# Performance work log

Hardware: AMD Instinct MI355X
Metric: run time of the kernel (lower is better)

## Reference

```python
import jax, jax.numpy as jnp
import numpy as np

N_NODES = 50000
D_IN = 128
D_OUT = 128
E_POS = 500000
E_NEG = 100000
BN_EPS = 1e-5


def setup_inputs() -> dict:
    key = jax.random.key(0)
    k = jax.random.split(key, 4)
    x = jax.random.normal(k[0], (N_NODES, D_IN), dtype=jnp.float32)
    pos_edge_index = jax.random.randint(k[1], (2, E_POS), 0, N_NODES, dtype=jnp.int64)
    neg_edge_index = jax.random.randint(k[2], (2, E_NEG), 0, N_NODES, dtype=jnp.int64)
    W = jax.random.normal(k[3], (D_IN, D_OUT), dtype=jnp.float32) * 0.05
    b = jnp.zeros((D_OUT,), dtype=jnp.float32)
    gamma = jnp.ones((D_OUT,), dtype=jnp.float32)
    beta = jnp.zeros((D_OUT,), dtype=jnp.float32)
    return {"x": x, "pos_edge_index": pos_edge_index, "neg_edge_index": neg_edge_index,
            "W": W, "b": b, "gamma": gamma, "beta": beta}


def reference(x, pos_edge_index, neg_edge_index, W, b, gamma, beta):
    N = x.shape[0]
    # edge weights: 1 for pos edges, 0 for neg edges (as in the torch module)
    ei = jnp.concatenate([pos_edge_index, neg_edge_index], axis=1)
    w = jnp.concatenate([jnp.ones((pos_edge_index.shape[1],), x.dtype),
                         jnp.zeros((neg_edge_index.shape[1],), x.dtype)])
    # GCNConv gcn_norm: add self-loops with weight 1.0
    loop = jnp.arange(N)
    row = jnp.concatenate([ei[0], loop])
    col = jnp.concatenate([ei[1], loop])
    w = jnp.concatenate([w, jnp.ones((N,), x.dtype)])
    # symmetric degree normalization over target (col)
    deg = jax.ops.segment_sum(w, col, num_segments=N)
    dis = jnp.where(deg > 0, jax.lax.rsqrt(jnp.maximum(deg, 1e-12)), 0.0)
    norm = dis[row] * w * dis[col]  # [E_total]
    # linear transform first, then scatter-add aggregation at col
    h = x @ W  # [N, D_OUT]
    out = jax.ops.segment_sum(norm[:, None] * h[row], col, num_segments=N) + b
    # BatchNorm1d (training mode, biased batch var) + ReLU
    mean = out.mean(axis=0)
    var = out.var(axis=0)
    xhat = (out - mean) * jax.lax.rsqrt(var + BN_EPS)
    return jax.nn.relu(gamma * xhat + beta)
```

## Files before the change

kernel.cpp:

```cpp
#include <hip/hip_runtime.h>

#define D 128
#define BN_EPS 1e-5f
#define K_ELL 40
#define NB_AGG 1024

__device__ __forceinline__ unsigned bf16rne(float f) {
    unsigned u = __float_as_uint(f);
    return (u + 0x7fffu + ((u >> 16) & 1u)) >> 16;
}
__device__ __forceinline__ float bflo(unsigned p) { return __uint_as_float(p << 16); }
__device__ __forceinline__ float bfhi(unsigned p) { return __uint_as_float(p & 0xffff0000u); }

__global__ void count_fill(const int* __restrict__ prow, const int* __restrict__ pcol,
                           int* __restrict__ deg, int* __restrict__ ell,
                           int2* __restrict__ ovf, int* __restrict__ ovf_cnt, int E) {
    int e = blockIdx.x * blockDim.x + threadIdx.x;
    if (e < E) {
        int c = pcol[e];
        int r = prow[e];
        int p = atomicAdd(&deg[c], 1);
        if (p < K_ELL) {
            ell[c * K_ELL + p] = r;
        } else {
            int q = atomicAdd(ovf_cnt, 1);
            ovf[q] = make_int2(c, r);
        }
    }
}

__global__ __launch_bounds__(256) void gemm_xw(const float* __restrict__ x,
                                               const float* __restrict__ W,
                                               const int* __restrict__ deg,
                                               float* __restrict__ dis,
                                               unsigned* __restrict__ hb, int n) {
    __shared__ float xs[32][68];
    __shared__ float ws[32][128];
    int tid = threadIdx.x;
    int tx = tid & 31;
    int ty = tid >> 5;
    int row0 = blockIdx.x * 64;

    if (tid < 64) {
        int gr = row0 + tid;
        if (gr < n) dis[gr] = rsqrtf((float)deg[gr] + 1.0f);
    }

    float acc[8][4] = {};
    for (int k0 = 0; k0 < 128; k0 += 32) {
        #pragma unroll
        for (int i = 0; i < 2; i++) {
            int li = tid + i * 256;
            int r = li >> 3;
            int kq = li & 7;
            int grow = row0 + r;
            if (grow >= n) grow = n - 1;
            float4 v = *(const float4*)&x[(size_t)grow * D + k0 + kq * 4];
            xs[kq * 4 + 0][r] = v.x;
            xs[kq * 4 + 1][r] = v.y;
            xs[kq * 4 + 2][r] = v.z;
            xs[kq * 4 + 3][r] = v.w;
        }
        #pragma unroll
        for (int i = 0; i < 4; i++) {
            int li = tid + i * 256;
            int c4 = li & 31;
            int k = li >> 5;
            *(float4*)&ws[k][c4 * 4] = *(const float4*)&W[(size_t)(k0 + k) * D + c4 * 4];
        }
        __syncthreads();
        #pragma unroll
        for (int k = 0; k < 32; k++) {
            float4 wv = *(const float4*)&ws[k][tx * 4];
            float xr[8];
            *(float4*)&xr[0] = *(const float4*)&xs[k][ty * 8];
            *(float4*)&xr[4] = *(const float4*)&xs[k][ty * 8 + 4];
            #pragma unroll
            for (int r = 0; r < 8; r++) {
                acc[r][0] += xr[r] * wv.x;
                acc[r][1] += xr[r] * wv.y;
                acc[r][2] += xr[r] * wv.z;
                acc[r][3] += xr[r] * wv.w;
            }
        }
        __syncthreads();
    }
    #pragma unroll
    for (int r = 0; r < 8; r++) {
        int gr = row0 + ty * 8 + r;
        if (gr < n) {
            uint2 pk;
            pk.x = bf16rne(acc[r][0]) | (bf16rne(acc[r][1]) << 16);
            pk.y = bf16rne(acc[r][2]) | (bf16rne(acc[r][3]) << 16);
            *(uint2*)&hb[(size_t)gr * 64 + tx * 2] = pk;
        }
    }
}

__global__ __launch_bounds__(512) void aggregate(const unsigned* __restrict__ hb,
                                                 const float* __restrict__ dis,
                                                 const int* __restrict__ deg,
                                                 const int* __restrict__ ell,
                                                 const int2* __restrict__ ovf,
                                                 const int* __restrict__ ovf_cnt,
                                                 const float* __restrict__ bias,
                                                 float* __restrict__ out,
                                                 float* __restrict__ partials, int n) {
    int tid = threadIdx.x;
    int wave = tid >> 6;
    int lane = tid & 63;
    float2 bv = *(const float2*)&bias[lane * 2];
    float s1a = 0.f, s1b = 0.f, s2a = 0.f, s2b = 0.f;

    for (int node = blockIdx.x * 8 + wave; node < n; node += gridDim.x * 8) {
        float dc = dis[node];
        int cntT = deg[node];
        int cntE = cntT < K_ELL ? cntT : K_ELL;
        unsigned hp = hb[(size_t)node * 64 + lane];
        float ax = dc * bflo(hp), ay = dc * bfhi(hp);
        int es = (lane < cntE) ? ell[node * K_ELL + lane] : 0;
        float ed = (lane < cntE) ? dis[es] : 0.f;
        int e = 0;
        for (; e + 4 <= cntE; e += 4) {
            int sA = __shfl(es, e), sB = __shfl(es, e + 1);
            int sC = __shfl(es, e + 2), sD = __shfl(es, e + 3);
            float dA = __shfl(ed, e), dB = __shfl(ed, e + 1);
            float dC = __shfl(ed, e + 2), dD = __shfl(ed, e + 3);
            unsigned hA = hb[(size_t)sA * 64 + lane];
            unsigned hB = hb[(size_t)sB * 64 + lane];
            unsigned hC = hb[(size_t)sC * 64 + lane];
            unsigned hD = hb[(size_t)sD * 64 + lane];
            ax += dA * bflo(hA); ay += dA * bfhi(hA);
            ax += dB * bflo(hB); ay += dB * bfhi(hB);
            ax += dC * bflo(hC); ay += dC * bfhi(hC);
            ax += dD * bflo(hD); ay += dD * bfhi(hD);
        }
        for (; e < cntE; e++) {
            int s = __shfl(es, e);
            float dv = __shfl(ed, e);
            unsigned hq = hb[(size_t)s * 64 + lane];
            ax += dv * bflo(hq); ay += dv * bfhi(hq);
        }
        if (cntT > K_ELL) {
            int novf = *ovf_cnt;
            for (int j = 0; j < novf; j++) {
                int2 q = ovf[j];
                if (q.x == node) {
                    float dv = dis[q.y];
                    unsigned hq = hb[(size_t)q.y * 64 + lane];
                    ax += dv * bflo(hq); ay += dv * bfhi(hq);
                }
            }
        }
        float ox = dc * ax + bv.x;
        float oy = dc * ay + bv.y;
        *(float2*)&out[(size_t)node * D + lane * 2] = make_float2(ox, oy);
        s1a += ox; s1b += oy;
        s2a += ox * ox; s2b += oy * oy;
    }

    __shared__ float l1[8][128], l2[8][128];
    l1[wave][lane * 2] = s1a; l1[wave][lane * 2 + 1] = s1b;
    l2[wave][lane * 2] = s2a; l2[wave][lane * 2 + 1] = s2b;
    __syncthreads();
    if (tid < 256) {
        int col = tid & 127;
        float v;
        if (tid < 128) {
            v = l1[0][col] + l1[1][col] + l1[2][col] + l1[3][col] +
                l1[4][col] + l1[5][col] + l1[6][col] + l1[7][col];
        } else {
            v = l2[0][col] + l2[1][col] + l2[2][col] + l2[3][col] +
                l2[4][col] + l2[5][col] + l2[6][col] + l2[7][col];
        }
        partials[(size_t)blockIdx.x * 256 + tid] = v;
    }
}

__global__ __launch_bounds__(256) void bn_reduce(const float* __restrict__ partials,
                                                 float* __restrict__ gsum,
                                                 float* __restrict__ gsumsq, int nrows) {
    int tid = threadIdx.x;
    float s = 0.f;
    for (int r = blockIdx.x; r < nrows; r += gridDim.x)
        s += partials[(size_t)r * 256 + tid];
    if (tid < 128) atomicAdd(&gsum[tid], s);
    else           atomicAdd(&gsumsq[tid - 128], s);
}

__global__ __launch_bounds__(256) void bn_finalize(float4* __restrict__ out4,
                                                   const float* __restrict__ gsum,
                                                   const float* __restrict__ gsumsq,
                                                   const float* __restrict__ gamma,
                                                   const float* __restrict__ beta,
                                                   int total4, float invN) {
    int i0 = blockIdx.x * 256 + threadIdx.x;
    int c = (i0 * 4) & 127;
    float4 g4 = *(const float4*)&gsum[c];
    float4 q4 = *(const float4*)&gsumsq[c];
    float4 gm = *(const float4*)&gamma[c];
    float4 bt = *(const float4*)&beta[c];
    float m0 = g4.x * invN, m1 = g4.y * invN, m2 = g4.z * invN, m3 = g4.w * invN;
    float sc0 = rsqrtf(q4.x * invN - m0 * m0 + BN_EPS) * gm.x;
    float sc1 = rsqrtf(q4.y * invN - m1 * m1 + BN_EPS) * gm.y;
    float sc2 = rsqrtf(q4.z * invN - m2 * m2 + BN_EPS) * gm.z;
    float sc3 = rsqrtf(q4.w * invN - m3 * m3 + BN_EPS) * gm.w;
    float sh0 = bt.x - m0 * sc0, sh1 = bt.y - m1 * sc1;
    float sh2 = bt.z - m2 * sc2, sh3 = bt.w - m3 * sc3;
    for (int i = i0; i < total4; i += gridDim.x * 256) {
        float4 v = out4[i];
        v.x = fmaxf(fmaf(v.x, sc0, sh0), 0.f);
        v.y = fmaxf(fmaf(v.y, sc1, sh1), 0.f);
        v.z = fmaxf(fmaf(v.z, sc2, sh2), 0.f);
        v.w = fmaxf(fmaf(v.w, sc3, sh3), 0.f);
        out4[i] = v;
    }
}

extern "C" void kernel_launch(void* const* d_in, const int* in_sizes, int n_in,
                              void* d_out, int out_size, void* d_ws, size_t ws_size,
                              hipStream_t stream) {
    const float* x     = (const float*)d_in[0];
    const int*   pos   = (const int*)d_in[1];
    const float* W     = (const float*)d_in[3];
    const float* bias  = (const float*)d_in[4];
    const float* gamma = (const float*)d_in[5];
    const float* beta  = (const float*)d_in[6];
    float* out = (float*)d_out;

    int N  = in_sizes[0] / D;
    int EP = in_sizes[1] / 2;
    const int* prow = pos;
    const int* pcol = pos + EP;

    auto align = [](size_t v) { return (v + 255) & ~(size_t)255; };
    char* p = (char*)d_ws;
    int*      deg     = (int*)p;      p += align((size_t)N * 4);
    int*      ovf_cnt = (int*)p;      p += align(256);
    float*    gsum    = (float*)p;    p += align((size_t)D * 4);
    float*    gsumsq  = (float*)p;    p += align((size_t)D * 4);
    size_t zbytes = (size_t)(p - (char*)d_ws);
    float*    dis      = (float*)p;    p += align((size_t)N * 4);
    int*      ell      = (int*)p;      p += align((size_t)N * K_ELL * 4);
    int2*     ovf      = (int2*)p;     p += align((size_t)EP * 8);
    unsigned* hb       = (unsigned*)p; p += align((size_t)N * 64 * 4);
    float*    partials = (float*)p;    p += align((size_t)NB_AGG * 256 * 4);

    hipMemsetAsync(d_ws, 0, zbytes, stream);
    count_fill<<<(EP + 255) / 256, 256, 0, stream>>>(prow, pcol, deg, ell, ovf, ovf_cnt, EP);
    gemm_xw<<<(N + 63) / 64, 256, 0, stream>>>(x, W, deg, dis, hb, N);
    aggregate<<<NB_AGG, 512, 0, stream>>>(hb, dis, deg, ell, ovf, ovf_cnt, bias, out,
                                          partials, N);
    bn_reduce<<<64, 256, 0, stream>>>(partials, gsum, gsumsq, NB_AGG);
    bn_finalize<<<1600, 256, 0, stream>>>((float4*)out, gsum, gsumsq, gamma, beta,
                                          N * D / 4, 1.0f / (float)N);
}
```

Before: 178.8 us.

## Use bf16 MFMA for the X·W GEMM and compute degree norms on the fly

Replaces the FP32 SIMT tiled GEMM with a bf16 MFMA kernel (16x16x32), using W pre-converted and transposed to bf16 inside the edge-counting prep kernel. It drops the dis array and computes rsqrt(deg+1) inline in the aggregation kernel. The aim is to cut GEMM compute time and remove a dependency and a store. In exchange, x is rounded to bf16 before the multiply, which adds precision loss. The GEMM also writes scalar 16-bit stores, which coalesce less well than before.

```diff
diff --git a/kernel.cpp b/kernel.cpp
--- a/kernel.cpp
+++ b/kernel.cpp
@@ -5,6 +5,9 @@
 #define K_ELL 40
 #define NB_AGG 1024
 
+typedef __attribute__((ext_vector_type(8))) short bf16x8;
+typedef __attribute__((ext_vector_type(4))) float f32x4;
+
 __device__ __forceinline__ unsigned bf16rne(float f) {
     unsigned u = __float_as_uint(f);
     return (u + 0x7fffu + ((u >> 16) & 1u)) >> 16;
@@ -12,11 +15,17 @@
 __device__ __forceinline__ float bflo(unsigned p) { return __uint_as_float(p << 16); }
 __device__ __forceinline__ float bfhi(unsigned p) { return __uint_as_float(p & 0xffff0000u); }
 
-__global__ void count_fill(const int* __restrict__ prow, const int* __restrict__ pcol,
-                           int* __restrict__ deg, int* __restrict__ ell,
-                           int2* __restrict__ ovf, int* __restrict__ ovf_cnt, int E) {
-    int e = blockIdx.x * blockDim.x + threadIdx.x;
-    if (e < E) {
+__global__ void prep(const int* __restrict__ prow, const int* __restrict__ pcol,
+                     int* __restrict__ deg, int* __restrict__ ell,
+                     int2* __restrict__ ovf, int* __restrict__ ovf_cnt,
+                     const float* __restrict__ W, ushort* __restrict__ wbT, int E) {
+    int gtid = blockIdx.x * blockDim.x + threadIdx.x;
+    int gsz = gridDim.x * blockDim.x;
+    for (int i = gtid; i < D * D; i += gsz) {
+        int k = i >> 7, c = i & 127;
+        wbT[c * D + k] = (ushort)bf16rne(W[i]);
+    }
+    for (int e = gtid; e < E; e += gsz) {
         int c = pcol[e];
         int r = prow[e];
         int p = atomicAdd(&deg[c], 1);
@@ -29,76 +38,80 @@
     }
 }
 
-__global__ __launch_bounds__(256) void gemm_xw(const float* __restrict__ x,
-                                               const float* __restrict__ W,
-                                               const int* __restrict__ deg,
-                                               float* __restrict__ dis,
-                                               unsigned* __restrict__ hb, int n) {
-    __shared__ float xs[32][68];
-    __shared__ float ws[32][128];
+__global__ __launch_bounds__(256) void gemm_mfma(const float* __restrict__ x,
+                                                 const ushort* __restrict__ wbT,
+                                                 ushort* __restrict__ hb, int n) {
+    __shared__ ushort xsb[64][136];
+    __shared__ ushort wsb[128][136];
     int tid = threadIdx.x;
-    int tx = tid & 31;
-    int ty = tid >> 5;
+    int wave = tid >> 6;
+    int lane = tid & 63;
     int row0 = blockIdx.x * 64;
 
-    if (tid < 64) {
-        int gr = row0 + tid;
-        if (gr < n) dis[gr] = rsqrtf((float)deg[gr] + 1.0f);
-    }
-
-    float acc[8][4] = {};
+    #pragma unroll
+    for (int i = 0; i < 8; i++) {
+        int flat = i * 256 + tid;
+        int c = flat >> 4, seg = flat & 15;
+        *(uint4*)&wsb[c][seg * 8] = ((const uint4*)wbT)[flat];
+    }
+    {
+        int r = tid >> 2, kq = tid & 3;
+        int grow = row0 + r;
+        if (grow >= n) grow = n - 1;
+        const float4* src = (const float4*)&x[(size_t)grow * D + kq * 32];
+        uint* dst = (uint*)&xsb[r][kq * 32];
+        #pragma unroll
+        for (int q = 0; q < 8; q++) {
+            float4 v = src[q];
+            dst[q * 2]     = bf16rne(v.x) | (bf16rne(v.y) << 16);
+            dst[q * 2 + 1] = bf16rne(v.z) | (bf16rne(v.w) << 16);
+        }
+    }
+    __syncthreads();
+
+    f32x4 acc[4][2];
+    #pragma unroll
+    for (int mt = 0; mt < 4; mt++)
+        #pragma unroll
+        for (int nt = 0; nt < 2; nt++)
+            acc[mt][nt] = (f32x4){0.f, 0.f, 0.f, 0.f};
+
+    int ar = lane & 15;
+    int ako = (lane >> 4) * 8;
+    #pragma unroll
     for (int k0 = 0; k0 < 128; k0 += 32) {
-        #pragma unroll
-        for (int i = 0; i < 2; i++) {
-            int li = tid + i * 256;
-            int r = li >> 3;
-            int kq = li & 7;
-            int grow = row0 + r;
-            if (grow >= n) grow = n - 1;
-            float4 v = *(const float4*)&x[(size_t)grow * D + k0 + kq * 4];
-            xs[kq * 4 + 0][r] = v.x;
-            xs[kq * 4 + 1][r] = v.y;
-            xs[kq * 4 + 2][r] = v.z;
-            xs[kq * 4 + 3][r] = v.w;
-        }
-        #pragma unroll
-        for (int i = 0; i < 4; i++) {
-            int li = tid + i * 256;
-            int c4 = li & 31;
-            int k = li >> 5;
-            *(float4*)&ws[k][c4 * 4] = *(const float4*)&W[(size_t)(k0 + k) * D + c4 * 4];
-        }
-        __syncthreads();
-        #pragma unroll
-        for (int k = 0; k < 32; k++) {
-            float4 wv = *(const float4*)&ws[k][tx * 4];
-            float xr[8];
-            *(float4*)&xr[0] = *(const float4*)&xs[k][ty * 8];
-            *(float4*)&xr[4] = *(const float4*)&xs[k][ty * 8 + 4];
+        bf16x8 a[4], b[2];
+        #pragma unroll
+        for (int mt = 0; mt < 4; mt++)
+            a[mt] = *(const bf16x8*)&xsb[mt * 16 + ar][k0 + ako];
+        #pragma unroll
+        for (int nt = 0; nt < 2; nt++)
+            b[nt] = *(const bf16x8*)&wsb[wave * 32 + nt * 16 + ar][k0 + ako];
+        #pragma unroll
+        for (int mt = 0; mt < 4; mt++)
             #pragma unroll
-            for (int r = 0; r < 8; r++) {
-                acc[r][0] += xr[r] * wv.x;
-                acc[r][1] += xr[r] * wv.y;
-                acc[r][2] += xr[r] * wv.z;
-                acc[r][3] += xr[r] * wv.w;
+            for (int nt = 0; nt < 2; nt++)
+                acc[mt][nt] = __builtin_amdgcn_mfma_f32_16x16x32_bf16(
+                    a[mt], b[nt], acc[mt][nt], 0, 0, 0);
+    }
+
+    int col = lane & 15, rq = (lane >> 4) * 4;
+    #pragma unroll
+    for (int mt = 0; mt < 4; mt++) {
+        #pragma unroll
+        for (int r = 0; r < 4; r++) {
+            int grow = row0 + mt * 16 + rq + r;
+            if (grow < n) {
+                #pragma unroll
+                for (int nt = 0; nt < 2; nt++)
+                    hb[(size_t)grow * D + wave * 32 + nt * 16 + col] =
+                        (ushort)bf16rne(acc[mt][nt][r]);
             }
         }
-        __syncthreads();
-    }
-    #pragma unroll
-    for (int r = 0; r < 8; r++) {
-        int gr = row0 + ty * 8 + r;
-        if (gr < n) {
-            uint2 pk;
-            pk.x = bf16rne(acc[r][0]) | (bf16rne(acc[r][1]) << 16);
-            pk.y = bf16rne(acc[r][2]) | (bf16rne(acc[r][3]) << 16);
-            *(uint2*)&hb[(size_t)gr * 64 + tx * 2] = pk;
-        }
     }
 }
 
 __global__ __launch_bounds__(512) void aggregate(const unsigned* __restrict__ hb,
-                                                 const float* __restrict__ dis,
                                                  const int* __restrict__ deg,
                                                  const int* __restrict__ ell,
                                                  const int2* __restrict__ ovf,
@@ -113,13 +126,13 @@
     float s1a = 0.f, s1b = 0.f, s2a = 0.f, s2b = 0.f;
 
     for (int node = blockIdx.x * 8 + wave; node < n; node += gridDim.x * 8) {
-        float dc = dis[node];
         int cntT = deg[node];
+        float dc = rsqrtf((float)cntT + 1.0f);
         int cntE = cntT < K_ELL ? cntT : K_ELL;
         unsigned hp = hb[(size_t)node * 64 + lane];
         float ax = dc * bflo(hp), ay = dc * bfhi(hp);
         int es = (lane < cntE) ? ell[node * K_ELL + lane] : 0;
-        float ed = (lane < cntE) ? dis[es] : 0.f;
+        float ed = (lane < cntE) ? rsqrtf((float)deg[es] + 1.0f) : 0.f;
         int e = 0;
         for (; e + 4 <= cntE; e += 4) {
             int sA = __shfl(es, e), sB = __shfl(es, e + 1);
@@ -146,7 +159,7 @@
             for (int j = 0; j < novf; j++) {
                 int2 q = ovf[j];
                 if (q.x == node) {
-                    float dv = dis[q.y];
+                    float dv = rsqrtf((float)deg[q.y] + 1.0f);
                     unsigned hq = hb[(size_t)q.y * 64 + lane];
                     ax += dv * bflo(hq); ay += dv * bfhi(hq);
                 }
@@ -240,17 +253,18 @@
     float*    gsum    = (float*)p;    p += align((size_t)D * 4);
     float*    gsumsq  = (float*)p;    p += align((size_t)D * 4);
     size_t zbytes = (size_t)(p - (char*)d_ws);
-    float*    dis      = (float*)p;    p += align((size_t)N * 4);
+    ushort*   wbT      = (ushort*)p;   p += align((size_t)D * D * 2);
     int*      ell      = (int*)p;      p += align((size_t)N * K_ELL * 4);
     int2*     ovf      = (int2*)p;     p += align((size_t)EP * 8);
-    unsigned* hb       = (unsigned*)p; p += align((size_t)N * 64 * 4);
+    ushort*   hb       = (ushort*)p;   p += align((size_t)N * D * 2);
     float*    partials = (float*)p;    p += align((size_t)NB_AGG * 256 * 4);
 
     hipMemsetAsync(d_ws, 0, zbytes, stream);
-    count_fill<<<(EP + 255) / 256, 256, 0, stream>>>(prow, pcol, deg, ell, ovf, ovf_cnt, EP);
-    gemm_xw<<<(N + 63) / 64, 256, 0, stream>>>(x, W, deg, dis, hb, N);
-    aggregate<<<NB_AGG, 512, 0, stream>>>(hb, dis, deg, ell, ovf, ovf_cnt, bias, out,
-                                          partials, N);
+    prep<<<(EP + 255) / 256, 256, 0, stream>>>(prow, pcol, deg, ell, ovf, ovf_cnt,
+                                               W, wbT, EP);
+    gemm_mfma<<<(N + 63) / 64, 256, 0, stream>>>(x, wbT, hb, N);
+    aggregate<<<NB_AGG, 512, 0, stream>>>((const unsigned*)hb, deg, ell, ovf, ovf_cnt,
+                                          bias, out, partials, N);
     bn_reduce<<<64, 256, 0, stream>>>(partials, gsum, gsumsq, NB_AGG);
     bn_finalize<<<1600, 256, 0, stream>>>((float4*)out, gsum, gsumsq, gamma, beta,
                                           N * D / 4, 1.0f / (float)N);
```

After: 158.7 us. 11.2% less time.
